# Optimization experiments

Hardware: AMD Instinct MI355X
Metric: run time of the kernel (lower is better)

Reference implementation:

```python
import jax, jax.numpy as jnp
import numpy as np

HIDDEN = 4096
N_HEADS = 32
QK_NOPE = 128
QK_ROPE = 64
QK_HEAD = QK_NOPE + QK_ROPE  # 192
V_HEAD = 128
Q_LORA = 1536
KV_LORA = 512
EPS = 1e-6
ROPE_BASE = 10000.0
T = 2048


def rmsnorm(x, g, eps=EPS):
    var = jnp.mean(x * x, axis=-1, keepdims=True)
    return x * jax.lax.rsqrt(var + eps) * g


def apply_rope_interleaved(x, cos, sin):
    # non-neox style: rotate interleaved pairs. x: [T, ..., d]; cos/sin: [T, d//2]
    x1 = x[..., 0::2]
    x2 = x[..., 1::2]
    while cos.ndim < x1.ndim:
        cos = cos[:, None]
        sin = sin[:, None]
    o1 = x1 * cos - x2 * sin
    o2 = x1 * sin + x2 * cos
    return jnp.stack([o1, o2], axis=-1).reshape(x.shape)


def setup_inputs() -> dict:
    key = jax.random.key(0)
    ks = jax.random.split(key, 8)
    s = lambda fan_in: 1.0 / np.sqrt(fan_in)
    return {
        "positions": jnp.arange(T, dtype=jnp.int32),
        "hidden_states": jax.random.normal(ks[0], (T, HIDDEN), jnp.float32),
        "wq_a": jax.random.normal(ks[1], (HIDDEN, Q_LORA), jnp.float32) * s(HIDDEN),
        "gq": jnp.ones((Q_LORA,), jnp.float32),
        "wq_b": jax.random.normal(ks[2], (Q_LORA, N_HEADS * QK_HEAD), jnp.float32) * s(Q_LORA),
        "wkv_a": jax.random.normal(ks[3], (HIDDEN, KV_LORA + QK_ROPE), jnp.float32) * s(HIDDEN),
        "gkv": jnp.ones((KV_LORA,), jnp.float32),
        "wkv_b": jax.random.normal(ks[4], (KV_LORA, N_HEADS * (QK_NOPE + V_HEAD)), jnp.float32) * s(KV_LORA),
        "wo": jax.random.normal(ks[5], (N_HEADS * V_HEAD, HIDDEN), jnp.float32) * s(N_HEADS * V_HEAD),
    }


def reference(positions, hidden_states, wq_a, gq, wq_b, wkv_a, gkv, wkv_b, wo):
    t = hidden_states.shape[0]
    scale = QK_HEAD ** -0.5

    # Q path: low-rank down-proj -> RMSNorm -> up-proj
    q = rmsnorm(hidden_states @ wq_a, gq) @ wq_b  # [T, H*192]
    q = q.reshape(t, N_HEADS, QK_HEAD)
    q_nope, q_pe = q[..., :QK_NOPE], q[..., QK_NOPE:]

    # KV path: compressed latent + decoupled rope key
    kv_a = hidden_states @ wkv_a  # [T, kv_lora + rope]
    c_kv, k_pe = kv_a[:, :KV_LORA], kv_a[:, KV_LORA:]
    kv = rmsnorm(c_kv, gkv) @ wkv_b  # [T, H*(nope+v)]
    kv = kv.reshape(t, N_HEADS, QK_NOPE + V_HEAD)
    k_nope, v = kv[..., :QK_NOPE], kv[..., QK_NOPE:]

    # RoPE (interleaved / non-neox)
    inv_freq = 1.0 / (ROPE_BASE ** (jnp.arange(0, QK_ROPE, 2, dtype=jnp.float32) / QK_ROPE))
    angles = positions.astype(jnp.float32)[:, None] * inv_freq[None, :]  # [T, rope/2]
    cos, sin = jnp.cos(angles), jnp.sin(angles)
    q_pe = apply_rope_interleaved(q_pe, cos, sin)          # [T, H, rope]
    k_pe = apply_rope_interleaved(k_pe, cos, sin)          # [T, rope]

    q_full = jnp.concatenate([q_nope, q_pe], axis=-1)       # [T, H, 192]
    k_full = jnp.concatenate(
        [k_nope, jnp.broadcast_to(k_pe[:, None, :], (t, N_HEADS, QK_ROPE))], axis=-1)

    scores = jnp.einsum('qhd,khd->hqk', q_full, k_full) * scale  # [H, T, T]
    causal = positions[:, None] >= positions[None, :]
    scores = jnp.where(causal[None], scores, jnp.finfo(scores.dtype).min)
    probs = jax.nn.softmax(scores, axis=-1)
    attn = jnp.einsum('hqk,khd->qhd', probs, v)              # [T, H, 128]
    return attn.reshape(t, N_HEADS * V_HEAD) @ wo            # [T, hidden]
```

## Files before the change

### kernel.cpp

```cpp
#include <hip/hip_runtime.h>
#include <hip/hip_bf16.h>
#include <stdint.h>

typedef __hip_bfloat16 bf16;
typedef unsigned short u16;
typedef short v8s __attribute__((ext_vector_type(8)));
typedef float v4f __attribute__((ext_vector_type(4)));

#define T_LEN   2048
#define HIDDEN  4096
#define N_HEADS 32
#define QK_NOPE 128
#define QK_ROPE 64
#define QK_HEAD 192
#define V_HEAD  128
#define Q_LORA  1536
#define KV_LORA 512
#define NFUSE   2176

enum { DT_BF16 = 0, DT_F32 = 1, DT_EXT = 2 };

__device__ __forceinline__ u16 f2b(float x) {
    union { bf16 h; u16 u; } cv; cv.h = __float2bfloat16(x); return cv.u;
}

typedef const __attribute__((address_space(1))) uint32_t* gas_ptr;
typedef __attribute__((address_space(3))) uint32_t* las_ptr;
__device__ __forceinline__ void gll16(const void* g, void* l) {
    __builtin_amdgcn_global_load_lds((gas_ptr)g, (las_ptr)l, 16, 0, 0);
}

__global__ __launch_bounds__(256) void convert_bf16(
    const void* __restrict__ X, u16* __restrict__ Y, int nelem,
    const uint32_t* __restrict__ probe)
{
    const bool f32 = (probe[0] & 0xFFFFu) == 0u;
    const int i = (blockIdx.x * 256 + threadIdx.x) * 8;
    if (i >= nelem) return;
    if (f32) {
        const float* x = (const float*)X + i;
        u16 o[8];
        #pragma unroll
        for (int e = 0; e < 8; ++e) o[e] = f2b(x[e]);
        *(uint4*)(Y + i) = *(const uint4*)o;
    } else {
        *(uint4*)(Y + i) = *(const uint4*)((const u16*)X + i);
    }
}

__global__ __launch_bounds__(256) void transpose_to_bf16(
    const void* __restrict__ W, u16* __restrict__ Wt,
    int K, int N, const uint32_t* __restrict__ probe)
{
    const bool f32 = (probe[0] & 0xFFFFu) == 0u;
    __shared__ uint32_t Ts[64 * 33];
    const int n0 = blockIdx.x * 64;
    const int k0 = blockIdx.y * 64;
    const int tid = threadIdx.x;
    {
        const int nc = (tid & 7) * 8;
        const int kp = tid >> 3;
        const int k = k0 + kp * 2;
        uint32_t vals[8];
        if (n0 >= N) {
            #pragma unroll
            for (int e = 0; e < 8; ++e) vals[e] = 0;
        } else if (f32) {
            const float* w0 = (const float*)W + (size_t)k * N + n0 + nc;
            const float* w1 = w0 + N;
            #pragma unroll
            for (int e = 0; e < 8; ++e)
                vals[e] = (uint32_t)f2b(w0[e]) | ((uint32_t)f2b(w1[e]) << 16);
        } else {
            const u16* w0 = (const u16*)W + (size_t)k * N + n0 + nc;
            const u16* w1 = w0 + N;
            u16 a[8], b[8];
            *(uint4*)a = *(const uint4*)w0;
            *(uint4*)b = *(const uint4*)w1;
            #pragma unroll
            for (int e = 0; e < 8; ++e)
                vals[e] = (uint32_t)a[e] | ((uint32_t)b[e] << 16);
        }
        #pragma unroll
        for (int e = 0; e < 8; ++e)
            Ts[(nc + e) * 33 + kp] = vals[e];
    }
    __syncthreads();
    {
        const int n = tid >> 2;
        const int kp0 = (tid & 3) * 8;
        u16 out[16];
        #pragma unroll
        for (int j = 0; j < 8; ++j) {
            const uint32_t v = Ts[n * 33 + kp0 + j];
            out[2 * j]     = (u16)(v & 0xFFFFu);
            out[2 * j + 1] = (u16)(v >> 16);
        }
        u16* dst = Wt + (size_t)(n0 + n) * K + k0 + kp0 * 2;
        *(uint4*)dst = *(const uint4*)out;
        *(uint4*)(dst + 8) = *(const uint4*)(out + 8);
    }
}

__global__ __launch_bounds__(256) void gemm_bt(
    const u16* __restrict__ A, const u16* __restrict__ Bt,
    void* __restrict__ C, int ccode,
    int N, int K, const uint32_t* __restrict__ probe)
{
    __shared__ __align__(16) u16 As[128 * 32];
    __shared__ __align__(16) u16 Bs[128 * 32];

    const int tid  = threadIdx.x;
    const int lane = tid & 63;
    const int wave = tid >> 6;
    const int quad = lane >> 4, l15 = lane & 15;
    const int wr = (wave >> 1) * 64, wc = (wave & 1) * 64;
    const size_t brow = (size_t)blockIdx.y * 128;
    const size_t bcol = (size_t)blockIdx.x * 128;

    v4f acc[4][4];
    #pragma unroll
    for (int i = 0; i < 4; ++i)
        #pragma unroll
        for (int j = 0; j < 4; ++j)
            acc[i][j] = (v4f){0.f, 0.f, 0.f, 0.f};

    const int c0 = tid, c1 = tid + 256;
    const int r0 = c0 >> 2, e0 = (c0 & 3) * 8;
    const int r1 = c1 >> 2, e1 = (c1 & 3) * 8;
    const u16* Ab = A + brow * K;
    const u16* Bb = Bt + bcol * K;

    for (int k0 = 0; k0 < K; k0 += 32) {
        gll16(Ab + (size_t)r0 * K + k0 + e0, (void*)(As + c0 * 8));
        gll16(Ab + (size_t)r1 * K + k0 + e1, (void*)(As + c1 * 8));
        gll16(Bb + (size_t)r0 * K + k0 + e0, (void*)(Bs + c0 * 8));
        gll16(Bb + (size_t)r1 * K + k0 + e1, (void*)(Bs + c1 * 8));
        __syncthreads();

        v8s af[4], bf[4];
        #pragma unroll
        for (int i = 0; i < 4; ++i)
            af[i] = *(const v8s*)(As + (wr + i * 16 + l15) * 32 + quad * 8);
        #pragma unroll
        for (int j = 0; j < 4; ++j)
            bf[j] = *(const v8s*)(Bs + (wc + j * 16 + l15) * 32 + quad * 8);
        #pragma unroll
        for (int i = 0; i < 4; ++i)
            #pragma unroll
            for (int j = 0; j < 4; ++j)
                acc[i][j] = __builtin_amdgcn_mfma_f32_16x16x32_bf16(
                    af[i], bf[j], acc[i][j], 0, 0, 0);
        __syncthreads();
    }

    const bool c_f32 = (ccode == DT_F32) ||
                       (ccode == DT_EXT && (probe[0] & 0xFFFFu) == 0u);
    #pragma unroll
    for (int i = 0; i < 4; ++i) {
        #pragma unroll
        for (int r = 0; r < 4; ++r) {
            const size_t row = brow + wr + i * 16 + quad * 4 + r;
            #pragma unroll
            for (int j = 0; j < 4; ++j) {
                const size_t col = bcol + wc + j * 16 + l15;
                if (c_f32) ((float*)C)[row * N + col] = acc[i][j][r];
                else       ((u16*)C)[row * N + col]   = f2b(acc[i][j][r]);
            }
        }
    }
}

__global__ __launch_bounds__(256) void rmsnorm_kernel(
    const float* __restrict__ x, const void* __restrict__ g,
    bf16* __restrict__ y, int cols,
    const uint32_t* __restrict__ probe)
{
    const bool g_f32 = (probe[0] & 0xFFFFu) == 0u;
    const int row = blockIdx.x;
    const float* xr = x + (size_t)row * NFUSE;
    float ss = 0.f;
    for (int c = threadIdx.x; c < cols; c += 256) {
        float v = xr[c];
        ss += v * v;
    }
    #pragma unroll
    for (int off = 32; off > 0; off >>= 1) ss += __shfl_down(ss, off, 64);
    __shared__ float wsum[4];
    const int wave = threadIdx.x >> 6, lane = threadIdx.x & 63;
    if (lane == 0) wsum[wave] = ss;
    __syncthreads();
    const float tot = wsum[0] + wsum[1] + wsum[2] + wsum[3];
    const float inv = rsqrtf(tot / (float)cols + 1e-6f);
    for (int c = threadIdx.x; c < cols; c += 256) {
        const float gv = g_f32 ? ((const float*)g)[c]
                               : __bfloat162float(((const bf16*)g)[c]);
        y[(size_t)row * cols + c] = __float2bfloat16(xr[c] * inv * gv);
    }
}

__global__ void kpe_rope_kernel(const float* __restrict__ qkv,
                                const int* __restrict__ pos,
                                bf16* __restrict__ kpe)
{
    const int t = blockIdx.x;
    const int i = threadIdx.x;
    const float x1 = qkv[(size_t)t * NFUSE + 2048 + 2 * i];
    const float x2 = qkv[(size_t)t * NFUSE + 2048 + 2 * i + 1];
    const float inv_freq = powf(10000.f, -(float)(2 * i) / 64.f);
    const float ang = (float)pos[t] * inv_freq;
    float s, c;
    sincosf(ang, &s, &c);
    kpe[(size_t)t * 64 + 2 * i]     = __float2bfloat16(x1 * c - x2 * s);
    kpe[(size_t)t * 64 + 2 * i + 1] = __float2bfloat16(x1 * s + x2 * c);
}

__global__ __launch_bounds__(256) void qpe_rope_kernel(bf16* __restrict__ q,
                                                       const int* __restrict__ pos)
{
    const int idx = blockIdx.x * 256 + threadIdx.x;
    const int i = idx & 31;
    const int h = (idx >> 5) & 31;
    const int t = idx >> 10;
    if (t >= T_LEN) return;
    bf16* base = q + ((size_t)t * N_HEADS + h) * QK_HEAD + QK_NOPE + 2 * i;
    const float x1 = __bfloat162float(base[0]);
    const float x2 = __bfloat162float(base[1]);
    const float inv_freq = powf(10000.f, -(float)(2 * i) / 64.f);
    const float ang = (float)pos[t] * inv_freq;
    float s, c;
    sincosf(ang, &s, &c);
    base[0] = __float2bfloat16(x1 * c - x2 * s);
    base[1] = __float2bfloat16(x1 * s + x2 * c);
}

#define KS_LD 200
#define VT_LD 72
#define PS_LD 72

__global__ __launch_bounds__(256) void attn_mfma(
    const bf16* __restrict__ qg, const bf16* __restrict__ kvg,
    const bf16* __restrict__ kpeg, bf16* __restrict__ attng)
{
    __shared__ u16 Ks[64 * KS_LD];
    __shared__ u16 Vt[V_HEAD * VT_LD];
    __shared__ u16 Ps[4 * 32 * PS_LD];

    const int bx = blockIdx.x;
    const int h  = bx & 31;
    const int qt = 15 - (bx >> 5);
    const int q0 = qt * 128;
    const int nkt = 2 * qt + 2;

    const int tid  = threadIdx.x;
    const int wave = tid >> 6, lane = tid & 63;
    const int quad = lane >> 4, l15 = lane & 15;
    const float scale = 0.07216878364870323f;

    v8s qf[2][6];
    #pragma unroll
    for (int mi = 0; mi < 2; ++mi)
        #pragma unroll
        for (int ks = 0; ks < 6; ++ks)
            qf[mi][ks] = *(const v8s*)((const u16*)qg +
                (size_t)(q0 + wave * 32 + mi * 16 + l15) * 6144 +
                h * 192 + ks * 32 + quad * 8);

    v4f accO[2][8];
    #pragma unroll
    for (int mi = 0; mi < 2; ++mi)
        #pragma unroll
        for (int vs = 0; vs < 8; ++vs)
            accO[mi][vs] = (v4f){0.f, 0.f, 0.f, 0.f};
    float m_run[2][4], l_run[2][4];
    #pragma unroll
    for (int mi = 0; mi < 2; ++mi)
        #pragma unroll
        for (int r = 0; r < 4; ++r) { m_run[mi][r] = -1e30f; l_run[mi][r] = 0.f; }

    for (int kt = 0; kt < nkt; ++kt) {
        const int k0 = kt * 64;
        __syncthreads();
        {
            const int jj = tid >> 4;
            const int c0 = (tid & 15) * 16;
            #pragma unroll
            for (int p = 0; p < 4; ++p) {
                const int j = jj + p * 16;
                const u16* src = (const u16*)kvg +
                    (size_t)(k0 + j) * 8192 + h * 256 + c0;
                uint4 v0 = *(const uint4*)src;
                uint4 v1 = *(const uint4*)(src + 8);
                if (c0 < 128) {
                    u16* dst = &Ks[j * KS_LD + c0];
                    *(uint4*)dst = v0;
                    *(uint4*)(dst + 8) = v1;
                } else {
                    u16 buf[16];
                    *(uint4*)buf = v0;
                    *(uint4*)(buf + 8) = v1;
                    const int d0 = c0 - 128;
                    #pragma unroll
                    for (int e = 0; e < 16; ++e) {
                        const int d = d0 + e;
                        const int jswz = j ^ (((d >> 4) & 7) << 3);
                        Vt[d * VT_LD + jswz] = buf[e];
                    }
                }
            }
            const int j2 = tid >> 2;
            const int c2 = (tid & 3) * 16;
            const u16* src = (const u16*)kpeg + (size_t)(k0 + j2) * 64 + c2;
            uint4 w0 = *(const uint4*)src;
            uint4 w1 = *(const uint4*)(src + 8);
            u16* dst = &Ks[j2 * KS_LD + 128 + c2];
            *(uint4*)dst = w0;
            *(uint4*)(dst + 8) = w1;
        }
        __syncthreads();

        v4f accS[2][4];
        #pragma unroll
        for (int mi = 0; mi < 2; ++mi)
            #pragma unroll
            for (int nj = 0; nj < 4; ++nj)
                accS[mi][nj] = (v4f){0.f, 0.f, 0.f, 0.f};
        #pragma unroll
        for (int ks = 0; ks < 6; ++ks) {
            v8s kf[4];
            #pragma unroll
            for (int nj = 0; nj < 4; ++nj)
                kf[nj] = *(const v8s*)&Ks[(nj * 16 + l15) * KS_LD + ks * 32 + quad * 8];
            #pragma unroll
            for (int mi = 0; mi < 2; ++mi)
                #pragma unroll
                for (int nj = 0; nj < 4; ++nj)
                    accS[mi][nj] = __builtin_amdgcn_mfma_f32_16x16x32_bf16(
                        qf[mi][ks], kf[nj], accS[mi][nj], 0, 0, 0);
        }

        const bool need_mask = (kt >= 2 * qt);
        float p[2][4][4];
        float alpha[2][4];
        #pragma unroll
        for (int mi = 0; mi < 2; ++mi) {
            #pragma unroll
            for (int r = 0; r < 4; ++r) {
                const int qrow = q0 + wave * 32 + mi * 16 + quad * 4 + r;
                float sv[4];
                float rm = -1e30f;
                #pragma unroll
                for (int nj = 0; nj < 4; ++nj) {
                    float s = accS[mi][nj][r] * scale;
                    if (need_mask) {
                        const int jgl = k0 + nj * 16 + l15;
                        if (jgl > qrow) s = -1e30f;
                    }
                    sv[nj] = s;
                    rm = fmaxf(rm, s);
                }
                rm = fmaxf(rm, __shfl_xor(rm, 1));
                rm = fmaxf(rm, __shfl_xor(rm, 2));
                rm = fmaxf(rm, __shfl_xor(rm, 4));
                rm = fmaxf(rm, __shfl_xor(rm, 8));
                const float mo = m_run[mi][r];
                const float mn = fmaxf(mo, rm);
                const float al = __expf(mo - mn);
                float ps = 0.f;
                #pragma unroll
                for (int nj = 0; nj < 4; ++nj) {
                    const float pv = __expf(sv[nj] - mn);
                    p[mi][nj][r] = pv;
                    ps += pv;
                }
                ps += __shfl_xor(ps, 1);
                ps += __shfl_xor(ps, 2);
                ps += __shfl_xor(ps, 4);
                ps += __shfl_xor(ps, 8);
                l_run[mi][r] = l_run[mi][r] * al + ps;
                m_run[mi][r] = mn;
                alpha[mi][r] = al;
            }
        }

        #pragma unroll
        for (int mi = 0; mi < 2; ++mi)
            #pragma unroll
            for (int vs = 0; vs < 8; ++vs)
                #pragma unroll
                for (int r = 0; r < 4; ++r)
                    accO[mi][vs][r] *= alpha[mi][r];

        u16* psw = &Ps[wave * 32 * PS_LD];
        #pragma unroll
        for (int mi = 0; mi < 2; ++mi)
            #pragma unroll
            for (int nj = 0; nj < 4; ++nj)
                #pragma unroll
                for (int r = 0; r < 4; ++r)
                    psw[(mi * 16 + quad * 4 + r) * PS_LD + nj * 16 + l15] =
                        f2b(p[mi][nj][r]);

        #pragma unroll
        for (int kf = 0; kf < 2; ++kf) {
            v8s pf[2];
            #pragma unroll
            for (int mi = 0; mi < 2; ++mi)
                pf[mi] = *(const v8s*)&psw[(mi * 16 + l15) * PS_LD + kf * 32 + quad * 8];
            #pragma unroll
            for (int vs = 0; vs < 8; ++vs) {
                const int swz = (vs & 7) << 3;
                v8s vf = *(const v8s*)&Vt[(vs * 16 + l15) * VT_LD +
                                          ((kf * 32 + quad * 8) ^ swz)];
                #pragma unroll
                for (int mi = 0; mi < 2; ++mi)
                    accO[mi][vs] = __builtin_amdgcn_mfma_f32_16x16x32_bf16(
                        pf[mi], vf, accO[mi][vs], 0, 0, 0);
            }
        }
    }

    #pragma unroll
    for (int mi = 0; mi < 2; ++mi) {
        #pragma unroll
        for (int r = 0; r < 4; ++r) {
            const int qrow = q0 + wave * 32 + mi * 16 + quad * 4 + r;
            const float linv = 1.f / l_run[mi][r];
            #pragma unroll
            for (int vs = 0; vs < 8; ++vs)
                attng[(size_t)qrow * 4096 + h * 128 + vs * 16 + l15] =
                    __float2bfloat16(accO[mi][vs][r] * linv);
        }
    }
}

extern "C" void kernel_launch(void* const* d_in, const int* in_sizes, int n_in,
                              void* d_out, int out_size, void* d_ws, size_t ws_size,
                              hipStream_t stream)
{
    const int*  pos    = (const int*)d_in[0];
    const void* hidden = d_in[1];
    const void* wq_a   = d_in[2];
    const void* gq     = d_in[3];
    const void* wq_b   = d_in[4];
    const void* wkv_a  = d_in[5];
    const void* gkv    = d_in[6];
    const void* wkv_b  = d_in[7];
    const void* wo     = d_in[8];
    const uint32_t* probe = (const uint32_t*)gq;

    char* w = (char*)d_ws;
    u16*   h_bf   = (u16*)w;   w += (size_t)T_LEN * HIDDEN * 2;
    u16*   Wt_qkv = (u16*)w;   w += (size_t)NFUSE * HIDDEN * 2;
    u16*   Wt_qb  = (u16*)w;   w += (size_t)6144 * Q_LORA * 2;
    u16*   Wt_kvb = (u16*)w;   w += (size_t)8192 * KV_LORA * 2;
    u16*   Wt_o   = (u16*)w;   w += (size_t)HIDDEN * HIDDEN * 2;
    float* qkv    = (float*)w; w += (size_t)T_LEN * NFUSE * 4;
    u16*   q_norm = (u16*)w;   w += (size_t)T_LEN * Q_LORA * 2;
    u16*   q      = (u16*)w;   w += (size_t)T_LEN * N_HEADS * QK_HEAD * 2;
    u16*   ckv    = (u16*)w;   w += (size_t)T_LEN * KV_LORA * 2;
    u16*   kpe    = (u16*)w;   w += (size_t)T_LEN * QK_ROPE * 2;
    u16*   kv     = (u16*)w;   w += (size_t)T_LEN * N_HEADS * 256 * 2;
    u16*   attn   = Wt_qkv;

    convert_bf16<<<4096, 256, 0, stream>>>(hidden, h_bf, T_LEN * HIDDEN, probe);
    transpose_to_bf16<<<dim3(1536 / 64, HIDDEN / 64), 256, 0, stream>>>(
        wq_a, Wt_qkv, HIDDEN, 1536, probe);
    transpose_to_bf16<<<dim3(640 / 64, HIDDEN / 64), 256, 0, stream>>>(
        wkv_a, Wt_qkv + (size_t)1536 * HIDDEN, HIDDEN, 576, probe);
    transpose_to_bf16<<<dim3(6144 / 64, Q_LORA / 64), 256, 0, stream>>>(
        wq_b, Wt_qb, Q_LORA, 6144, probe);
    transpose_to_bf16<<<dim3(8192 / 64, KV_LORA / 64), 256, 0, stream>>>(
        wkv_b, Wt_kvb, KV_LORA, 8192, probe);
    transpose_to_bf16<<<dim3(HIDDEN / 64, HIDDEN / 64), 256, 0, stream>>>(
        wo, Wt_o, HIDDEN, HIDDEN, probe);

    gemm_bt<<<dim3(NFUSE / 128, T_LEN / 128), 256, 0, stream>>>(
        h_bf, Wt_qkv, qkv, DT_F32, NFUSE, HIDDEN, probe);

    rmsnorm_kernel<<<T_LEN, 256, 0, stream>>>(qkv, gq, (bf16*)q_norm, Q_LORA, probe);
    rmsnorm_kernel<<<T_LEN, 256, 0, stream>>>(qkv + 1536, gkv, (bf16*)ckv, KV_LORA, probe);
    kpe_rope_kernel<<<T_LEN, 32, 0, stream>>>(qkv, pos, (bf16*)kpe);

    gemm_bt<<<dim3(6144 / 128, T_LEN / 128), 256, 0, stream>>>(
        q_norm, Wt_qb, q, DT_BF16, 6144, Q_LORA, probe);
    qpe_rope_kernel<<<(T_LEN * N_HEADS * 32) / 256, 256, 0, stream>>>((bf16*)q, pos);

    gemm_bt<<<dim3(8192 / 128, T_LEN / 128), 256, 0, stream>>>(
        ckv, Wt_kvb, kv, DT_BF16, 8192, KV_LORA, probe);

    attn_mfma<<<dim3(N_HEADS * (T_LEN / 128)), 256, 0, stream>>>(
        (const bf16*)q, (const bf16*)kv, (const bf16*)kpe, (bf16*)attn);

    gemm_bt<<<dim3(HIDDEN / 128, T_LEN / 128), 256, 0, stream>>>(
        attn, Wt_o, d_out, DT_EXT, HIDDEN, HIDDEN, probe);
}
```

Before: 735.4 us.

## Prefetch next KV tile into registers, reorder block schedule, raise MFMA priority

The attention kernel now issues the global loads for the next K/V tile into registers right after the shared-memory store barrier, so they overlap with the current tile's MFMA work. The grid mapping changes so the second half of the blocks walks query tiles in ascending order instead of descending. s_setprio is raised around the MFMA loops to favour the matrix-core waves. The register prefetch buffers add register pressure, which could lower occupancy.

New measurement: 787.6 us. +7.1%, slower.

```diff
diff --git a/kernel.cpp b/kernel.cpp
--- a/kernel.cpp
+++ b/kernel.cpp
@@ -248,7 +248,8 @@
 
     const int bx = blockIdx.x;
     const int h  = bx & 31;
-    const int qt = 15 - (bx >> 5);
+    const int g  = bx >> 5;
+    const int qt = (bx < 256) ? (15 - g) : (g - 8);
     const int q0 = qt * 128;
     const int nkt = 2 * qt + 2;
 
@@ -278,46 +279,63 @@
         #pragma unroll
         for (int r = 0; r < 4; ++r) { m_run[mi][r] = -1e30f; l_run[mi][r] = 0.f; }
 
+    const int jj = tid >> 4;
+    const int c0 = (tid & 15) * 16;
+    const int j2 = tid >> 2;
+    const int c2 = (tid & 3) * 16;
+
+    uint4 kvb[4][2];
+    uint4 kpb[2];
+
+    auto load_tile = [&](int k0n) {
+        #pragma unroll
+        for (int p = 0; p < 4; ++p) {
+            const int j = jj + p * 16;
+            const u16* src = (const u16*)kvg +
+                (size_t)(k0n + j) * 8192 + h * 256 + c0;
+            kvb[p][0] = *(const uint4*)src;
+            kvb[p][1] = *(const uint4*)(src + 8);
+        }
+        const u16* s2 = (const u16*)kpeg + (size_t)(k0n + j2) * 64 + c2;
+        kpb[0] = *(const uint4*)s2;
+        kpb[1] = *(const uint4*)(s2 + 8);
+    };
+
+    auto store_tile = [&]() {
+        #pragma unroll
+        for (int p = 0; p < 4; ++p) {
+            const int j = jj + p * 16;
+            if (c0 < 128) {
+                u16* dst = &Ks[j * KS_LD + c0];
+                *(uint4*)dst = kvb[p][0];
+                *(uint4*)(dst + 8) = kvb[p][1];
+            } else {
+                u16 buf[16];
+                *(uint4*)buf = kvb[p][0];
+                *(uint4*)(buf + 8) = kvb[p][1];
+                const int d0 = c0 - 128;
+                #pragma unroll
+                for (int e = 0; e < 16; ++e) {
+                    const int d = d0 + e;
+                    const int jswz = j ^ (((d >> 4) & 7) << 3);
+                    Vt[d * VT_LD + jswz] = buf[e];
+                }
+            }
+        }
+        u16* dst = &Ks[j2 * KS_LD + 128 + c2];
+        *(uint4*)dst = kpb[0];
+        *(uint4*)(dst + 8) = kpb[1];
+    };
+
+    load_tile(0);
+
     for (int kt = 0; kt < nkt; ++kt) {
         const int k0 = kt * 64;
         __syncthreads();
-        {
-            const int jj = tid >> 4;
-            const int c0 = (tid & 15) * 16;
-            #pragma unroll
-            for (int p = 0; p < 4; ++p) {
-                const int j = jj + p * 16;
-                const u16* src = (const u16*)kvg +
-                    (size_t)(k0 + j) * 8192 + h * 256 + c0;
-                uint4 v0 = *(const uint4*)src;
-                uint4 v1 = *(const uint4*)(src + 8);
-                if (c0 < 128) {
-                    u16* dst = &Ks[j * KS_LD + c0];
-                    *(uint4*)dst = v0;
-                    *(uint4*)(dst + 8) = v1;
-                } else {
-                    u16 buf[16];
-                    *(uint4*)buf = v0;
-                    *(uint4*)(buf + 8) = v1;
-                    const int d0 = c0 - 128;
-                    #pragma unroll
-                    for (int e = 0; e < 16; ++e) {
-                        const int d = d0 + e;
-                        const int jswz = j ^ (((d >> 4) & 7) << 3);
-                        Vt[d * VT_LD + jswz] = buf[e];
-                    }
-                }
-            }
-            const int j2 = tid >> 2;
-            const int c2 = (tid & 3) * 16;
-            const u16* src = (const u16*)kpeg + (size_t)(k0 + j2) * 64 + c2;
-            uint4 w0 = *(const uint4*)src;
-            uint4 w1 = *(const uint4*)(src + 8);
-            u16* dst = &Ks[j2 * KS_LD + 128 + c2];
-            *(uint4*)dst = w0;
-            *(uint4*)(dst + 8) = w1;
-        }
+        store_tile();
         __syncthreads();
+        if (kt + 1 < nkt)
+            load_tile((kt + 1) * 64);
 
         v4f accS[2][4];
         #pragma unroll
@@ -325,6 +343,7 @@
             #pragma unroll
             for (int nj = 0; nj < 4; ++nj)
                 accS[mi][nj] = (v4f){0.f, 0.f, 0.f, 0.f};
+        __builtin_amdgcn_s_setprio(1);
         #pragma unroll
         for (int ks = 0; ks < 6; ++ks) {
             v8s kf[4];
@@ -338,6 +357,7 @@
                     accS[mi][nj] = __builtin_amdgcn_mfma_f32_16x16x32_bf16(
                         qf[mi][ks], kf[nj], accS[mi][nj], 0, 0, 0);
         }
+        __builtin_amdgcn_s_setprio(0);
 
         const bool need_mask = (kt >= 2 * qt);
         float p[2][4][4];
@@ -401,6 +421,7 @@
                     psw[(mi * 16 + quad * 4 + r) * PS_LD + nj * 16 + l15] =
                         f2b(p[mi][nj][r]);
 
+        __builtin_amdgcn_s_setprio(1);
         #pragma unroll
         for (int kf = 0; kf < 2; ++kf) {
             v8s pf[2];
@@ -418,6 +439,7 @@
                         pf[mi], vf, accO[mi][vs], 0, 0, 0);
             }
         }
+        __builtin_amdgcn_s_setprio(0);
     }
 
     #pragma unroll
```
